# Optimization experiments

Hardware: AMD Instinct MI355X
Metric: run time of the kernel (lower is better)

## Reference

```python
import jax, jax.numpy as jnp
import numpy as np
import math

B, H, N, D = 2, 16, 8192, 64
NUM_PROJS = 7
BLOCK = 256   # key block size
SAMPLE = 256  # number of sampled columns


def _gray_perm(n):
    # AngularLSH._unit_hamming_distance_array: Gray-code ordering of 2**n buckets
    a = np.array([0, 1], dtype=np.int32)
    for i in range(1, n):
        a = np.concatenate([a, a[::-1] + 2 ** i])
    return a

PERM = jnp.asarray(_gray_perm(NUM_PROJS))
ENC = jnp.asarray(2 ** np.arange(NUM_PROJS), dtype=jnp.int32)


def lsh_hash(x, proj_dir):
    # sign-bit angular LSH, then Gray-code remap so nearby buckets share bits
    bits = (jnp.einsum('bhnd,dr->bhnr', x, proj_dir) > 0).astype(jnp.int32)
    bin_ids = (bits * ENC).sum(-1)
    return PERM[bin_ids]


def take_seq(x, idx):
    # gather along the sequence axis (axis=2); idx is [B,H,M]
    return jnp.take_along_axis(x, idx[..., None], axis=2)


def setup_inputs() -> dict:
    key = jax.random.key(0)
    ks = jax.random.split(key, 5)
    return {
        'query': jax.random.normal(ks[0], (B, H, N, D), jnp.float32),
        'key': jax.random.normal(ks[1], (B, H, N, D), jnp.float32),
        'value': jax.random.normal(ks[2], (B, H, N, D), jnp.float32),
        'proj_dir': jax.random.normal(ks[3], (D + 1, NUM_PROJS), jnp.float32),
        'sampled_set': jax.random.randint(ks[4], (B, H, SAMPLE), 0, N),
    }


def reference(query, key, value, proj_dir, sampled_set):
    scale = D ** -0.5

    # asymmetric MIPS transform: key gets sqrt(max||k||^2 - ||k||^2), query gets 0
    k_norm = jnp.linalg.norm(key, axis=-1)                 # [B,H,N]
    k_max = jnp.max(k_norm, axis=-1, keepdims=True)        # [B,H,1]
    k_extra = jnp.sqrt(jnp.maximum(k_max ** 2 - k_norm ** 2, 0.0))
    key_aug = jnp.concatenate([key, k_extra[..., None]], axis=-1)
    query_aug = jnp.concatenate([query, jnp.zeros_like(query[..., :1])], axis=-1)

    # stable sort by LSH bucket; inverse permutation to un-sort queries at the end
    q_idx = jnp.argsort(lsh_hash(query_aug, proj_dir), axis=2, stable=True)
    k_idx = jnp.argsort(lsh_hash(key_aug, proj_dir), axis=2, stable=True)
    q_idx_inv = jnp.argsort(q_idx, axis=2, stable=True)

    q_s = take_seq(query, q_idx)
    k_s = take_seq(key, k_idx)
    v_s = take_seq(value, k_idx)

    nb = N // BLOCK      # number of key blocks (N divisible by BLOCK here)
    qbs = N // nb        # query block size

    # 1) block-diagonal exact attention over LSH-sorted blocks
    qb = q_s.reshape(B, H, nb, qbs, D)
    kb = k_s.reshape(B, H, nb, BLOCK, D)
    vb = v_s.reshape(B, H, nb, BLOCK, D)
    s_blk = jnp.einsum('bhgqd,bhgkd->bhgqk', qb, kb) * scale
    lse_blk = jax.nn.logsumexp(s_blk, axis=-1)             # [B,H,nb,qbs]
    attn_blk = jnp.einsum('bhgqk,bhgkd->bhgqd', jax.nn.softmax(s_blk, axis=-1), vb)
    attn_blk = attn_blk.reshape(B, H, N, D)
    lse_blk = lse_blk.reshape(B, H, N, 1)

    # 2) residual via uniformly sampled columns; mask out columns already in the
    #    query's own diagonal block to avoid double counting
    k_sub = take_seq(k_s, sampled_set)                     # [B,H,S,D]
    v_sub = take_seq(v_s, sampled_set)
    q_blk_id = jnp.arange(N) // qbs                        # [N]
    covered = q_blk_id[None, None, :, None] == (sampled_set // BLOCK)[:, :, None, :]
    bias = jnp.where(covered, jnp.finfo(q_s.dtype).min, 0.0)
    s_res = jnp.einsum('bhnd,bhsd->bhns', q_s, k_sub) * scale + bias
    # importance weight n_key/sample_size applied in log-space (approximate_unsampled)
    lse_res = jax.nn.logsumexp(s_res, axis=-1, keepdims=True) + math.log(N / SAMPLE)
    attn_res = jnp.einsum('bhns,bhsd->bhnd', jax.nn.softmax(s_res, axis=-1), v_sub)

    # add_self_attentions: merge the two softmax estimates in log-space
    c = 1.0 / (1.0 + jnp.exp(lse_res - lse_blk))
    attn = c * attn_blk + (1.0 - c) * attn_res

    # un-sort rows back to the original query order
    attn = take_seq(attn, q_idx_inv)
    return attn
```

## Files before the change

kernel.cpp:

```cpp
#include <hip/hip_runtime.h>
#include <hip/hip_bf16.h>
#include <math.h>

#define BD 2
#define HD 16
#define NSEQ 8192
#define DDIM 64
#define NPROJ 7
#define KBLK 256
#define NSAMP 256
#define NBH (BD*HD)
#define NB (NSEQ/KBLK)

typedef short bf16x8 __attribute__((ext_vector_type(8)));
typedef short bf16x4 __attribute__((ext_vector_type(4)));
typedef float f32x4 __attribute__((ext_vector_type(4)));

__device__ __forceinline__ unsigned int pk2bf(float a, float b) {
    union { __hip_bfloat162 h; unsigned int u; } t;
    t.h = __float22bfloat162_rn(make_float2(a, b));
    return t.u;
}

__global__ __launch_bounds__(256) void prelude_kernel(const float* __restrict__ q,
                                                      const float* __restrict__ k,
                                                      const float* __restrict__ pd,
                                                      float* __restrict__ kdots,
                                                      unsigned int* __restrict__ kmax_bits,
                                                      unsigned char* __restrict__ qh) {
    __shared__ float pds[(DDIM+1)*NPROJ];
    __shared__ float red[256];
    const int tid = threadIdx.x;
    for (int i = tid; i < (DDIM+1)*NPROJ; i += 256) pds[i] = pd[i];
    __syncthreads();

    const int lin = blockIdx.x * 256 + tid;
    const int bh = lin >> 13;

    float acc[NPROJ];
    float4 xv[16];

    {
        const float4* xp = (const float4*)(q + (size_t)lin * DDIM);
        #pragma unroll
        for (int j = 0; j < 16; ++j) xv[j] = xp[j];
        #pragma unroll
        for (int r = 0; r < NPROJ; ++r) acc[r] = 0.f;
        #pragma unroll
        for (int j = 0; j < 16; ++j) {
            float xs[4] = {xv[j].x, xv[j].y, xv[j].z, xv[j].w};
            #pragma unroll
            for (int c = 0; c < 4; ++c) {
                const int d = j*4 + c;
                #pragma unroll
                for (int r = 0; r < NPROJ; ++r) acc[r] += xs[c] * pds[d*NPROJ + r];
            }
        }
        int bin = 0;
        #pragma unroll
        for (int r = 0; r < NPROJ; ++r) bin |= (acc[r] > 0.f) << r;
        qh[lin] = (unsigned char)(bin ^ (bin >> 1));
    }

    float nr;
    {
        const float4* xp = (const float4*)(k + (size_t)lin * DDIM);
        #pragma unroll
        for (int j = 0; j < 16; ++j) xv[j] = xp[j];
        #pragma unroll
        for (int r = 0; r < NPROJ; ++r) acc[r] = 0.f;
        #pragma unroll
        for (int j = 0; j < 16; ++j) {
            float xs[4] = {xv[j].x, xv[j].y, xv[j].z, xv[j].w};
            #pragma unroll
            for (int c = 0; c < 4; ++c) {
                const int d = j*4 + c;
                #pragma unroll
                for (int r = 0; r < NPROJ; ++r) acc[r] += xs[c] * pds[d*NPROJ + r];
            }
        }
        float ss = 0.f;
        #pragma unroll
        for (int j = 0; j < 16; ++j) {
            float4 t = xv[j];
            ss += t.x*t.x + t.y*t.y + t.z*t.z + t.w*t.w;
        }
        nr = sqrtf(ss);
        float4* kd = (float4*)(kdots + (size_t)lin * 8);
        kd[0] = make_float4(acc[0], acc[1], acc[2], acc[3]);
        kd[1] = make_float4(acc[4], acc[5], acc[6], nr);
    }

    red[tid] = nr;
    __syncthreads();
    for (int s = 128; s > 0; s >>= 1) {
        if (tid < s) red[tid] = fmaxf(red[tid], red[tid+s]);
        __syncthreads();
    }
    if (tid == 0) atomicMax(&kmax_bits[bh], __float_as_uint(red[0]));
}

__global__ __launch_bounds__(256) void khash_kernel(const float* __restrict__ pd,
                                                    const float* __restrict__ kdots,
                                                    const unsigned int* __restrict__ kmax_bits,
                                                    unsigned char* __restrict__ kh) {
    const int lin = blockIdx.x * 256 + threadIdx.x;
    const int bh = lin >> 13;
    const float4* kd = (const float4*)(kdots + (size_t)lin * 8);
    float4 d0 = kd[0], d1 = kd[1];
    float acc[NPROJ] = {d0.x, d0.y, d0.z, d0.w, d1.x, d1.y, d1.z};
    const float kn = d1.w;
    const float km = __uint_as_float(kmax_bits[bh]);
    const float ex = sqrtf(fmaxf(km*km - kn*kn, 0.f));
    int bin = 0;
    #pragma unroll
    for (int r = 0; r < NPROJ; ++r) {
        acc[r] += ex * pd[DDIM*NPROJ + r];
        bin |= (acc[r] > 0.f) << r;
    }
    kh[lin] = (unsigned char)(bin ^ (bin >> 1));
}

__global__ __launch_bounds__(256) void sort_kernel(const unsigned char* __restrict__ qhash,
                                                   const unsigned char* __restrict__ khash,
                                                   int* __restrict__ qidx,
                                                   int* __restrict__ kidx) {
    __shared__ unsigned char hsh[NSEQ];
    __shared__ unsigned short cnt[128][264];
    __shared__ int base[128];
    __shared__ int wtot[2];
    const int bh = blockIdx.x, tid = threadIdx.x;
    const unsigned char* hash = blockIdx.y ? khash : qhash;
    int* idx = blockIdx.y ? kidx : qidx;

    {
        const uint4* src = (const uint4*)(hash + (size_t)bh * NSEQ);
        uint4* hdst = (uint4*)hsh;
        hdst[tid] = src[tid];
        hdst[tid + 256] = src[tid + 256];
        unsigned int* cz = (unsigned int*)&cnt[0][0];
        for (int i = tid; i < 128*264/2; i += 256) cz[i] = 0;
    }
    __syncthreads();
    {
        const unsigned char* s = hsh + tid*32;
        for (int i = 0; i < 32; ++i) cnt[s[i]][tid]++;
    }
    __syncthreads();

    int sc = 0, vv = 0;
    if (tid < 128) {
        unsigned run = 0;
        uint4* rp = (uint4*)cnt[tid];
        for (int wd = 0; wd < 32; ++wd) {
            uint4 x = rp[wd];
            unsigned v0 = x.x & 0xffffu, v1 = x.x >> 16;
            unsigned v2 = x.y & 0xffffu, v3 = x.y >> 16;
            unsigned v4 = x.z & 0xffffu, v5 = x.z >> 16;
            unsigned v6 = x.w & 0xffffu, v7 = x.w >> 16;
            unsigned p0 = run, p1 = p0+v0, p2 = p1+v1, p3 = p2+v2,
                     p4 = p3+v3, p5 = p4+v4, p6 = p5+v5, p7 = p6+v6;
            run = p7 + v7;
            x.x = p0 | (p1<<16); x.y = p2 | (p3<<16);
            x.z = p4 | (p5<<16); x.w = p6 | (p7<<16);
            rp[wd] = x;
        }
        vv = (int)run;
        sc = vv;
        #pragma unroll
        for (int d = 1; d < 64; d <<= 1) {
            int t = __shfl_up(sc, d, 64);
            if ((tid & 63) >= d) sc += t;
        }
        if ((tid & 63) == 63) wtot[tid >> 6] = sc;
    }
    __syncthreads();
    if (tid < 128) base[tid] = (sc - vv) + (tid >= 64 ? wtot[0] : 0);
    __syncthreads();
    {
        int* dst = idx + (size_t)bh * NSEQ;
        const unsigned char* s = hsh + tid*32;
        for (int i = 0; i < 32; ++i) {
            int h = s[i];
            int c = cnt[h][tid];
            cnt[h][tid] = (unsigned short)(c + 1);
            dst[base[h] + c] = tid*32 + i;
        }
    }
}

#define VSWZ(d) ((((d) >> 1) & 7) << 4)

__global__ __launch_bounds__(256) void respack_kernel(const float* __restrict__ k,
                                                      const float* __restrict__ v,
                                                      const int* __restrict__ samp,
                                                      const int* __restrict__ kidx,
                                                      char* __restrict__ kres,
                                                      char* __restrict__ vres) {
    const int bh = blockIdx.x, ch = blockIdx.y, tid = threadIdx.x;
    const size_t basef = (size_t)bh * NSEQ * DDIM;
    char* kimg = kres + (size_t)(bh*4 + ch) * 8192;
    char* vimg = vres + (size_t)(bh*4 + ch) * 8192;

    {
        const int kk = tid & 63, dc = tid >> 6;
        const int sp = samp[bh*NSAMP + ch*64 + kk];
        const int row = kidx[bh*NSEQ + sp];
        const float* kr = k + basef + (size_t)row*DDIM + dc*16;
        float4 f0 = ((const float4*)kr)[0], f1 = ((const float4*)kr)[1];
        float4 f2 = ((const float4*)kr)[2], f3 = ((const float4*)kr)[3];
        union { bf16x8 v8; unsigned int u[4]; } h0, h1;
        h0.u[0] = pk2bf(f0.x,f0.y); h0.u[1] = pk2bf(f0.z,f0.w);
        h0.u[2] = pk2bf(f1.x,f1.y); h0.u[3] = pk2bf(f1.z,f1.w);
        h1.u[0] = pk2bf(f2.x,f2.y); h1.u[1] = pk2bf(f2.z,f2.w);
        h1.u[2] = pk2bf(f3.x,f3.y); h1.u[3] = pk2bf(f3.z,f3.w);
        const int rb = kk*128 + dc*32, sw = (kk & 7) << 4;
        *(bf16x8*)(kimg + ((rb) ^ sw)) = h0.v8;
        *(bf16x8*)(kimg + ((rb + 16) ^ sw)) = h1.v8;
    }
    {
        const int vg = tid & 15, kq = tid >> 4;
        const int r0 = kidx[bh*NSEQ + samp[bh*NSAMP + ch*64 + kq*4 + 0]];
        const int r1 = kidx[bh*NSEQ + samp[bh*NSAMP + ch*64 + kq*4 + 1]];
        const int r2 = kidx[bh*NSEQ + samp[bh*NSAMP + ch*64 + kq*4 + 2]];
        const int r3 = kidx[bh*NSEQ + samp[bh*NSAMP + ch*64 + kq*4 + 3]];
        float4 x0 = *(const float4*)(v + basef + (size_t)r0*DDIM + vg*4);
        float4 x1 = *(const float4*)(v + basef + (size_t)r1*DDIM + vg*4);
        float4 x2 = *(const float4*)(v + basef + (size_t)r2*DDIM + vg*4);
        float4 x3 = *(const float4*)(v + basef + (size_t)r3*DDIM + vg*4);
        const float c0[4] = {x0.x, x0.y, x0.z, x0.w};
        const float c1[4] = {x1.x, x1.y, x1.z, x1.w};
        const float c2[4] = {x2.x, x2.y, x2.z, x2.w};
        const float c3[4] = {x3.x, x3.y, x3.z, x3.w};
        #pragma unroll
        for (int j = 0; j < 4; ++j) {
            const int d = vg*4 + j;
            unsigned h01 = pk2bf(c0[j], c1[j]);
            unsigned h23 = pk2bf(c2[j], c3[j]);
            *(uint2*)(vimg + ((d*128 + kq*8) ^ VSWZ(d))) = make_uint2(h01, h23);
        }
    }
}


#define LN32 3.46573590279972f

template<int PHASE>
__device__ __forceinline__ void compute_chunk(
    int ch, int lane,
    const bf16x8 (&qhf)[4][2], const bf16x8 (&qlf)[4][2],
    f32x4 (&O)[4][4], float (&lacc)[4],
    const float* maskF, const char* KhL, const char* VthL) {

    const int lr4 = lane >> 4;
    const int lc  = lane & 15;

    #pragma unroll
    for (int mt = 0; mt < 4; ++mt) {
        const int key = mt*16 + lc;
        const int ksw = (key & 7) << 4;
        bf16x8 ka0 = *(const bf16x8*)(KhL + ((key*128 +  0 + lr4*16) ^ ksw));
        bf16x8 ka1 = *(const bf16x8*)(KhL + ((key*128 + 64 + lr4*16) ^ ksw));
        float4 mk;
        if (PHASE) mk = *(const float4*)(maskF + ch*64 + mt*16 + lr4*4);

        bf16x4 pb[4];
        #pragma unroll
        for (int qt = 0; qt < 4; ++qt) {
            f32x4 c = {0.f, 0.f, 0.f, 0.f};
            c = __builtin_amdgcn_mfma_f32_16x16x32_bf16(ka0, qhf[qt][0], c, 0, 0, 0);
            c = __builtin_amdgcn_mfma_f32_16x16x32_bf16(ka0, qlf[qt][0], c, 0, 0, 0);
            c = __builtin_amdgcn_mfma_f32_16x16x32_bf16(ka1, qhf[qt][1], c, 0, 0, 0);
            c = __builtin_amdgcn_mfma_f32_16x16x32_bf16(ka1, qlf[qt][1], c, 0, 0, 0);
            float e0, e1, e2, e3;
            if (PHASE) {
                e0 = __expf(c[0] + LN32) * mk.x;
                e1 = __expf(c[1] + LN32) * mk.y;
                e2 = __expf(c[2] + LN32) * mk.z;
                e3 = __expf(c[3] + LN32) * mk.w;
            } else {
                e0 = __expf(c[0]); e1 = __expf(c[1]);
                e2 = __expf(c[2]); e3 = __expf(c[3]);
            }
            lacc[qt] += (e0+e1) + (e2+e3);
            union { bf16x4 v4; unsigned int u[2]; } pw;
            pw.u[0] = pk2bf(e0, e1);
            pw.u[1] = pk2bf(e2, e3);
            pb[qt] = pw.v4;
        }

        __builtin_amdgcn_s_setprio(1);
        #pragma unroll
        for (int dt = 0; dt < 4; ++dt) {
            const int d = dt*16 + lc;
            bf16x4 va = *(const bf16x4*)(VthL + ((d*128 + mt*32 + lr4*8) ^ VSWZ(d)));
            #pragma unroll
            for (int qt = 0; qt < 4; ++qt)
                O[qt][dt] = __builtin_amdgcn_mfma_f32_16x16x16bf16_1k(va, pb[qt], O[qt][dt], 0, 0, 0);
        }
        __builtin_amdgcn_s_setprio(0);
    }
}

__global__ __launch_bounds__(256, 2) void attn_kernel(const float* __restrict__ q,
                                                      const float* __restrict__ k,
                                                      const float* __restrict__ v,
                                                      const int* __restrict__ samp,
                                                      const int* __restrict__ qidx,
                                                      const int* __restrict__ kidx,
                                                      const char* __restrict__ kres,
                                                      const char* __restrict__ vres,
                                                      float* __restrict__ out) {
    __shared__ __align__(16) char KB[8192];
    __shared__ __align__(16) char VB[8192];
    __shared__ int qidxL[256];
    __shared__ int kidxL[256];
    __shared__ float maskF[256];

    const int g = blockIdx.x, bh = blockIdx.y;
    const int tid = threadIdx.x;
    const int lane = tid & 63, w = tid >> 6;
    const int lr4 = lane >> 4, lc = lane & 15;
    const size_t basef = (size_t)bh * NSEQ * DDIM;

    qidxL[tid] = qidx[bh*NSEQ + g*KBLK + tid];
    kidxL[tid] = kidx[bh*NSEQ + g*KBLK + tid];
    {
        int sp = samp[bh*NSAMP + tid];
        maskF[tid] = ((sp >> 8) == g) ? 0.f : 1.f;
    }
    __syncthreads();

    bf16x8 qhf[4][2], qlf[4][2];
    #pragma unroll
    for (int qt = 0; qt < 4; ++qt) {
        const int qrow = qidxL[w*64 + qt*16 + lc];
        const float* qp = q + basef + (size_t)qrow*DDIM;
        #pragma unroll
        for (int ks = 0; ks < 2; ++ks) {
            const float* p = qp + ks*32 + lr4*8;
            float4 a = *(const float4*)p;
            float4 b = *(const float4*)(p + 4);
            float xs[8] = {a.x,a.y,a.z,a.w,b.x,b.y,b.z,b.w};
            union { bf16x8 v8; unsigned int u[4]; } hv, lv;
            #pragma unroll
            for (int j = 0; j < 4; ++j) {
                float s0 = xs[2*j]   * 0.125f;
                float s1 = xs[2*j+1] * 0.125f;
                unsigned hp = pk2bf(s0, s1);
                hv.u[j] = hp;
                float l0 = s0 - __uint_as_float(hp << 16);
                float l1 = s1 - __uint_as_float(hp & 0xffff0000u);
                lv.u[j] = pk2bf(l0, l1);
            }
            qhf[qt][ks] = hv.v8; qlf[qt][ks] = lv.v8;
        }
    }

    f32x4 O[4][4];
    #pragma unroll
    for (int a = 0; a < 4; ++a)
        #pragma unroll
        for (int b = 0; b < 4; ++b) O[a][b] = (f32x4){0.f,0.f,0.f,0.f};
    float lacc[4] = {0,0,0,0};

    const int kk = tid & 63, dcw = tid >> 6;
    const int vg = tid & 15, kq = tid >> 4;

    for (int ch = 0; ch < 4; ++ch) {
        __syncthreads();
        {
            const int korig = kidxL[ch*64 + kk];
            const float* kr = k + basef + (size_t)korig*DDIM + dcw*16;
            float4 f0 = ((const float4*)kr)[0], f1 = ((const float4*)kr)[1];
            float4 f2 = ((const float4*)kr)[2], f3 = ((const float4*)kr)[3];
            union { bf16x8 v8; unsigned int u[4]; } h0, h1;
            h0.u[0] = pk2bf(f0.x,f0.y); h0.u[1] = pk2bf(f0.z,f0.w);
            h0.u[2] = pk2bf(f1.x,f1.y); h0.u[3] = pk2bf(f1.z,f1.w);
            h1.u[0] = pk2bf(f2.x,f2.y); h1.u[1] = pk2bf(f2.z,f2.w);
            h1.u[2] = pk2bf(f3.x,f3.y); h1.u[3] = pk2bf(f3.z,f3.w);
            const int rb = kk*128 + dcw*32, sw2 = (kk & 7) << 4;
            *(bf16x8*)(KB + ((rb) ^ sw2)) = h0.v8;
            *(bf16x8*)(KB + ((rb + 16) ^ sw2)) = h1.v8;
        }
        {
            const int r0 = kidxL[ch*64 + kq*4 + 0];
            const int r1 = kidxL[ch*64 + kq*4 + 1];
            const int r2 = kidxL[ch*64 + kq*4 + 2];
            const int r3 = kidxL[ch*64 + kq*4 + 3];
            float4 x0 = *(const float4*)(v + basef + (size_t)r0*DDIM + vg*4);
            float4 x1 = *(const float4*)(v + basef + (size_t)r1*DDIM + vg*4);
            float4 x2 = *(const float4*)(v + basef + (size_t)r2*DDIM + vg*4);
            float4 x3 = *(const float4*)(v + basef + (size_t)r3*DDIM + vg*4);
            const float c0[4] = {x0.x, x0.y, x0.z, x0.w};
            const float c1[4] = {x1.x, x1.y, x1.z, x1.w};
            const float c2[4] = {x2.x, x2.y, x2.z, x2.w};
            const float c3[4] = {x3.x, x3.y, x3.z, x3.w};
            #pragma unroll
            for (int j = 0; j < 4; ++j) {
                const int d = vg*4 + j;
                unsigned h01 = pk2bf(c0[j], c1[j]);
                unsigned h23 = pk2bf(c2[j], c3[j]);
                *(uint2*)(VB + ((d*128 + kq*8) ^ VSWZ(d))) = make_uint2(h01, h23);
            }
        }
        __syncthreads();
        compute_chunk<0>(ch, lane, qhf, qlf, O, lacc, maskF, KB, VB);
    }

    for (int ch = 0; ch < 4; ++ch) {
        __syncthreads();
        {
            const char* ksrc = kres + (size_t)(bh*4 + ch) * 8192 + tid*32;
            const char* vsrc = vres + (size_t)(bh*4 + ch) * 8192 + tid*32;
            float4 a0 = ((const float4*)ksrc)[0];
            float4 a1 = ((const float4*)ksrc)[1];
            float4 b0 = ((const float4*)vsrc)[0];
            float4 b1 = ((const float4*)vsrc)[1];
            *(float4*)(KB + tid*32)      = a0;
            *(float4*)(KB + tid*32 + 16) = a1;
            *(float4*)(VB + tid*32)      = b0;
            *(float4*)(VB + tid*32 + 16) = b1;
        }
        __syncthreads();
        compute_chunk<1>(ch, lane, qhf, qlf, O, lacc, maskF, KB, VB);
    }

    #pragma unroll
    for (int qt = 0; qt < 4; ++qt) {
        lacc[qt] += __shfl_xor(lacc[qt], 16, 64);
        lacc[qt] += __shfl_xor(lacc[qt], 32, 64);
        lacc[qt] = 1.f / lacc[qt];
    }
    float* ob = out + basef;
    #pragma unroll
    for (int qt = 0; qt < 4; ++qt) {
        const int orow = qidxL[w*64 + qt*16 + lc];
        const float f = lacc[qt];
        float* p = ob + (size_t)orow*DDIM + lr4*4;
        #pragma unroll
        for (int dt = 0; dt < 4; ++dt) {
            float4 st = make_float4(O[qt][dt][0]*f, O[qt][dt][1]*f,
                                    O[qt][dt][2]*f, O[qt][dt][3]*f);
            *(float4*)(p + dt*16) = st;
        }
    }
}

extern "C" void kernel_launch(void* const* d_in, const int* in_sizes, int n_in,
                              void* d_out, int out_size, void* d_ws, size_t ws_size,
                              hipStream_t stream) {
    const float* q    = (const float*)d_in[0];
    const float* k    = (const float*)d_in[1];
    const float* v    = (const float*)d_in[2];
    const float* pd   = (const float*)d_in[3];
    const int*   samp = (const int*)d_in[4];
    float* out = (float*)d_out;

    char* ws = (char*)d_ws;
    float*         kdots = (float*)(ws + 0);
    int*           qidx  = (int*)(ws + 0);
    int*           kidx  = (int*)(ws + 1048576);
    char*          kres  = ws + 2097152;
    char*          vres  = ws + 3145728;
    unsigned char* qh    = (unsigned char*)(ws + 8388608);
    unsigned char* kh    = (unsigned char*)(ws + 8650752);
    unsigned int*  kmaxb = (unsigned int*)(ws + 8912896);

    hipMemsetAsync(kmaxb, 0, NBH*sizeof(unsigned int), stream);
    hipLaunchKernelGGL(prelude_kernel, dim3(NBH*NSEQ/256), dim3(256), 0, stream,
                       q, k, pd, kdots, kmaxb, qh);
    hipLaunchKernelGGL(khash_kernel, dim3(NBH*NSEQ/256), dim3(256), 0, stream,
                       pd, kdots, kmaxb, kh);
    hipLaunchKernelGGL(sort_kernel, dim3(NBH, 2), dim3(256), 0, stream, qh, kh, qidx, kidx);
    hipLaunchKernelGGL(respack_kernel, dim3(NBH, 4), dim3(256), 0, stream,
                       k, v, samp, kidx, kres, vres);
    hipLaunchKernelGGL(attn_kernel, dim3(NB, NBH), dim3(256), 0, stream,
                       q, k, v, samp, qidx, kidx, kres, vres, out);
}
```

Baseline: 157.5 us.

## Pre-pack sorted K/V into bf16 LDS images and double-buffer async loads

Adds a pack kernel that gathers the LSH-sorted K/V rows, converts them to bf16 and writes them in the swizzled LDS layout into a large workspace. A new attention kernel then streams these images, plus the residual images, into double-buffered shared memory with direct global-to-LDS loads, so the copy of the next chunk overlaps compute on the current one. The aim is to take the scattered gather and conversion out of the attention inner loop. The new path runs only when the workspace holds at least 84 MB, otherwise the old gather path runs. In exchange it adds a kernel launch and an extra full write and read of K/V, and the larger shared-memory footprint may reduce occupancy.

After: 285.8 us. +81.5%, slower.

```diff
diff --git a/kernel.cpp b/kernel.cpp
--- a/kernel.cpp
+++ b/kernel.cpp
@@ -20,6 +20,12 @@
     union { __hip_bfloat162 h; unsigned int u; } t;
     t.h = __float22bfloat162_rn(make_float2(a, b));
     return t.u;
+}
+
+__device__ __forceinline__ void gload16(const void* gsrc, void* lds) {
+    __builtin_amdgcn_global_load_lds(
+        (const __attribute__((address_space(1))) unsigned int*)gsrc,
+        (__attribute__((address_space(3))) unsigned int*)lds, 16, 0, 0);
 }
 
 __global__ __launch_bounds__(256) void prelude_kernel(const float* __restrict__ q,
@@ -191,55 +197,78 @@
 
 #define VSWZ(d) ((((d) >> 1) & 7) << 4)
 
+__device__ __forceinline__ void pack_k_chunk(const float* kbase, const int* rows,
+                                             int tid, char* kimg) {
+    const int kk = tid & 63, dc = tid >> 6;
+    const int row = rows[kk];
+    const float* kr = kbase + (size_t)row*DDIM + dc*16;
+    float4 f0 = ((const float4*)kr)[0], f1 = ((const float4*)kr)[1];
+    float4 f2 = ((const float4*)kr)[2], f3 = ((const float4*)kr)[3];
+    union { bf16x8 v8; unsigned int u[4]; } h0, h1;
+    h0.u[0] = pk2bf(f0.x,f0.y); h0.u[1] = pk2bf(f0.z,f0.w);
+    h0.u[2] = pk2bf(f1.x,f1.y); h0.u[3] = pk2bf(f1.z,f1.w);
+    h1.u[0] = pk2bf(f2.x,f2.y); h1.u[1] = pk2bf(f2.z,f2.w);
+    h1.u[2] = pk2bf(f3.x,f3.y); h1.u[3] = pk2bf(f3.z,f3.w);
+    const int rb = kk*128 + dc*32, sw = (kk & 7) << 4;
+    *(bf16x8*)(kimg + ((rb) ^ sw)) = h0.v8;
+    *(bf16x8*)(kimg + ((rb + 16) ^ sw)) = h1.v8;
+}
+
+__device__ __forceinline__ void pack_v_chunk(const float* vbase, const int* rows,
+                                             int tid, char* vimg) {
+    const int vg = tid & 15, kq = tid >> 4;
+    const int r0 = rows[kq*4 + 0];
+    const int r1 = rows[kq*4 + 1];
+    const int r2 = rows[kq*4 + 2];
+    const int r3 = rows[kq*4 + 3];
+    float4 x0 = *(const float4*)(vbase + (size_t)r0*DDIM + vg*4);
+    float4 x1 = *(const float4*)(vbase + (size_t)r1*DDIM + vg*4);
+    float4 x2 = *(const float4*)(vbase + (size_t)r2*DDIM + vg*4);
+    float4 x3 = *(const float4*)(vbase + (size_t)r3*DDIM + vg*4);
+    const float c0[4] = {x0.x, x0.y, x0.z, x0.w};
+    const float c1[4] = {x1.x, x1.y, x1.z, x1.w};
+    const float c2[4] = {x2.x, x2.y, x2.z, x2.w};
+    const float c3[4] = {x3.x, x3.y, x3.z, x3.w};
+    #pragma unroll
+    for (int j = 0; j < 4; ++j) {
+        const int d = vg*4 + j;
+        unsigned h01 = pk2bf(c0[j], c1[j]);
+        unsigned h23 = pk2bf(c2[j], c3[j]);
+        *(uint2*)(vimg + ((d*128 + kq*8) ^ VSWZ(d))) = make_uint2(h01, h23);
+    }
+}
+
+__global__ __launch_bounds__(256) void pack_kernel(const float* __restrict__ k,
+                                                   const float* __restrict__ v,
+                                                   const int* __restrict__ kidx,
+                                                   char* __restrict__ kimg,
+                                                   char* __restrict__ vimg) {
+    __shared__ int rows[64];
+    const int bh = blockIdx.x, cj = blockIdx.y, tid = threadIdx.x;
+    if (tid < 64) rows[tid] = kidx[bh*NSEQ + cj*64 + tid];
+    __syncthreads();
+    const size_t basef = (size_t)bh * NSEQ * DDIM;
+    char* kdst = kimg + (size_t)(bh*128 + cj) * 8192;
+    char* vdst = vimg + (size_t)(bh*128 + cj) * 8192;
+    pack_k_chunk(k + basef, rows, tid, kdst);
+    pack_v_chunk(v + basef, rows, tid, vdst);
+}
+
 __global__ __launch_bounds__(256) void respack_kernel(const float* __restrict__ k,
                                                       const float* __restrict__ v,
                                                       const int* __restrict__ samp,
                                                       const int* __restrict__ kidx,
                                                       char* __restrict__ kres,
                                                       char* __restrict__ vres) {
+    __shared__ int rows[64];
     const int bh = blockIdx.x, ch = blockIdx.y, tid = threadIdx.x;
+    if (tid < 64) rows[tid] = kidx[bh*NSEQ + samp[bh*NSAMP + ch*64 + tid]];
+    __syncthreads();
     const size_t basef = (size_t)bh * NSEQ * DDIM;
-    char* kimg = kres + (size_t)(bh*4 + ch) * 8192;
-    char* vimg = vres + (size_t)(bh*4 + ch) * 8192;
-
-    {
-        const int kk = tid & 63, dc = tid >> 6;
-        const int sp = samp[bh*NSAMP + ch*64 + kk];
-        const int row = kidx[bh*NSEQ + sp];
-        const float* kr = k + basef + (size_t)row*DDIM + dc*16;
-        float4 f0 = ((const float4*)kr)[0], f1 = ((const float4*)kr)[1];
-        float4 f2 = ((const float4*)kr)[2], f3 = ((const float4*)kr)[3];
-        union { bf16x8 v8; unsigned int u[4]; } h0, h1;
-        h0.u[0] = pk2bf(f0.x,f0.y); h0.u[1] = pk2bf(f0.z,f0.w);
-        h0.u[2] = pk2bf(f1.x,f1.y); h0.u[3] = pk2bf(f1.z,f1.w);
-        h1.u[0] = pk2bf(f2.x,f2.y); h1.u[1] = pk2bf(f2.z,f2.w);
-        h1.u[2] = pk2bf(f3.x,f3.y); h1.u[3] = pk2bf(f3.z,f3.w);
-        const int rb = kk*128 + dc*32, sw = (kk & 7) << 4;
-        *(bf16x8*)(kimg + ((rb) ^ sw)) = h0.v8;
-        *(bf16x8*)(kimg + ((rb + 16) ^ sw)) = h1.v8;
-    }
-    {
-        const int vg = tid & 15, kq = tid >> 4;
-        const int r0 = kidx[bh*NSEQ + samp[bh*NSAMP + ch*64 + kq*4 + 0]];
-        const int r1 = kidx[bh*NSEQ + samp[bh*NSAMP + ch*64 + kq*4 + 1]];
-        const int r2 = kidx[bh*NSEQ + samp[bh*NSAMP + ch*64 + kq*4 + 2]];
-        const int r3 = kidx[bh*NSEQ + samp[bh*NSAMP + ch*64 + kq*4 + 3]];
-        float4 x0 = *(const float4*)(v + basef + (size_t)r0*DDIM + vg*4);
-        float4 x1 = *(const float4*)(v + basef + (size_t)r1*DDIM + vg*4);
-        float4 x2 = *(const float4*)(v + basef + (size_t)r2*DDIM + vg*4);
-        float4 x3 = *(const float4*)(v + basef + (size_t)r3*DDIM + vg*4);
-        const float c0[4] = {x0.x, x0.y, x0.z, x0.w};
-        const float c1[4] = {x1.x, x1.y, x1.z, x1.w};
-        const float c2[4] = {x2.x, x2.y, x2.z, x2.w};
-        const float c3[4] = {x3.x, x3.y, x3.z, x3.w};
-        #pragma unroll
-        for (int j = 0; j < 4; ++j) {
-            const int d = vg*4 + j;
-            unsigned h01 = pk2bf(c0[j], c1[j]);
-            unsigned h23 = pk2bf(c2[j], c3[j]);
-            *(uint2*)(vimg + ((d*128 + kq*8) ^ VSWZ(d))) = make_uint2(h01, h23);
-        }
-    }
+    char* kdst = kres + (size_t)(bh*4 + ch) * 8192;
+    char* vdst = vres + (size_t)(bh*4 + ch) * 8192;
+    pack_k_chunk(k + basef, rows, tid, kdst);
+    pack_v_chunk(v + basef, rows, tid, vdst);
 }
 
 
@@ -302,36 +331,10 @@
     }
 }
 
-__global__ __launch_bounds__(256, 2) void attn_kernel(const float* __restrict__ q,
-                                                      const float* __restrict__ k,
-                                                      const float* __restrict__ v,
-                                                      const int* __restrict__ samp,
-                                                      const int* __restrict__ qidx,
-                                                      const int* __restrict__ kidx,
-                                                      const char* __restrict__ kres,
-                                                      const char* __restrict__ vres,
-                                                      float* __restrict__ out) {
-    __shared__ __align__(16) char KB[8192];
-    __shared__ __align__(16) char VB[8192];
-    __shared__ int qidxL[256];
-    __shared__ int kidxL[256];
-    __shared__ float maskF[256];
-
-    const int g = blockIdx.x, bh = blockIdx.y;
-    const int tid = threadIdx.x;
-    const int lane = tid & 63, w = tid >> 6;
+__device__ __forceinline__ void load_q_frags(const float* q, size_t basef,
+                                             const int* qidxL, int w, int lane,
+                                             bf16x8 (&qhf)[4][2], bf16x8 (&qlf)[4][2]) {
     const int lr4 = lane >> 4, lc = lane & 15;
-    const size_t basef = (size_t)bh * NSEQ * DDIM;
-
-    qidxL[tid] = qidx[bh*NSEQ + g*KBLK + tid];
-    kidxL[tid] = kidx[bh*NSEQ + g*KBLK + tid];
-    {
-        int sp = samp[bh*NSAMP + tid];
-        maskF[tid] = ((sp >> 8) == g) ? 0.f : 1.f;
-    }
-    __syncthreads();
-
-    bf16x8 qhf[4][2], qlf[4][2];
     #pragma unroll
     for (int qt = 0; qt < 4; ++qt) {
         const int qrow = qidxL[w*64 + qt*16 + lc];
@@ -356,6 +359,71 @@
             qhf[qt][ks] = hv.v8; qlf[qt][ks] = lv.v8;
         }
     }
+}
+
+__device__ __forceinline__ void write_out(float* out, size_t basef,
+                                          const int* qidxL, int w, int lane,
+                                          f32x4 (&O)[4][4], float (&lacc)[4]) {
+    const int lr4 = lane >> 4, lc = lane & 15;
+    #pragma unroll
+    for (int qt = 0; qt < 4; ++qt) {
+        lacc[qt] += __shfl_xor(lacc[qt], 16, 64);
+        lacc[qt] += __shfl_xor(lacc[qt], 32, 64);
+        lacc[qt] = 1.f / lacc[qt];
+    }
+    float* ob = out + basef;
+    #pragma unroll
+    for (int qt = 0; qt < 4; ++qt) {
+        const int orow = qidxL[w*64 + qt*16 + lc];
+        const float f = lacc[qt];
+        float* p = ob + (size_t)orow*DDIM + lr4*4;
+        #pragma unroll
+        for (int dt = 0; dt < 4; ++dt) {
+            float4 st = make_float4(O[qt][dt][0]*f, O[qt][dt][1]*f,
+                                    O[qt][dt][2]*f, O[qt][dt][3]*f);
+            *(float4*)(p + dt*16) = st;
+        }
+    }
+}
+
+__global__ __launch_bounds__(256, 2) void attn_kernel_img(const float* __restrict__ q,
+                                                          const int* __restrict__ samp,
+                                                          const int* __restrict__ qidx,
+                                                          const char* __restrict__ kimg,
+                                                          const char* __restrict__ vimg,
+                                                          const char* __restrict__ kres,
+                                                          const char* __restrict__ vres,
+                                                          float* __restrict__ out) {
+    __shared__ __align__(16) char KB[2][8192];
+    __shared__ __align__(16) char VB[2][8192];
+    __shared__ int qidxL[256];
+    __shared__ float maskF[256];
+
+    const int g = blockIdx.x, bh = blockIdx.y;
+    const int tid = threadIdx.x;
+    const int lane = tid & 63, w = tid >> 6;
+    const size_t basef = (size_t)bh * NSEQ * DDIM;
+
+    qidxL[tid] = qidx[bh*NSEQ + g*KBLK + tid];
+    {
+        int sp = samp[bh*NSAMP + tid];
+        maskF[tid] = ((sp >> 8) == g) ? 0.f : 1.f;
+    }
+
+    {
+        const char* ks = kimg + (size_t)(bh*128 + g*4) * 8192;
+        const char* vs = vimg + (size_t)(bh*128 + g*4) * 8192;
+        char* kl = KB[0] + w*1024;
+        char* vl = VB[0] + w*1024;
+        gload16(ks + tid*16, kl);
+        gload16(ks + 4096 + tid*16, kl + 4096);
+        gload16(vs + tid*16, vl);
+        gload16(vs + 4096 + tid*16, vl + 4096);
+    }
+    __syncthreads();
+
+    bf16x8 qhf[4][2], qlf[4][2];
+    load_q_frags(q, basef, qidxL, w, lane, qhf, qlf);
 
     f32x4 O[4][4];
     #pragma unroll
@@ -364,50 +432,73 @@
         for (int b = 0; b < 4; ++b) O[a][b] = (f32x4){0.f,0.f,0.f,0.f};
     float lacc[4] = {0,0,0,0};
 
-    const int kk = tid & 63, dcw = tid >> 6;
-    const int vg = tid & 15, kq = tid >> 4;
+    for (int ch = 0; ch < 8; ++ch) {
+        if (ch < 7) {
+            const int nch = ch + 1;
+            const char* ks = (nch < 4) ? kimg + (size_t)(bh*128 + g*4 + nch) * 8192
+                                       : kres + (size_t)(bh*4 + nch - 4) * 8192;
+            const char* vs = (nch < 4) ? vimg + (size_t)(bh*128 + g*4 + nch) * 8192
+                                       : vres + (size_t)(bh*4 + nch - 4) * 8192;
+            char* kl = KB[nch & 1] + w*1024;
+            char* vl = VB[nch & 1] + w*1024;
+            gload16(ks + tid*16, kl);
+            gload16(ks + 4096 + tid*16, kl + 4096);
+            gload16(vs + tid*16, vl);
+            gload16(vs + 4096 + tid*16, vl + 4096);
+        }
+        if (ch < 4) compute_chunk<0>(ch,   lane, qhf, qlf, O, lacc, maskF, KB[ch&1], VB[ch&1]);
+        else        compute_chunk<1>(ch-4, lane, qhf, qlf, O, lacc, maskF, KB[ch&1], VB[ch&1]);
+        __syncthreads();
+    }
+
+    write_out(out, basef, qidxL, w, lane, O, lacc);
+}
+
+__global__ __launch_bounds__(256, 2) void attn_kernel_gather(const float* __restrict__ q,
+                                                             const float* __restrict__ k,
+                                                             const float* __restrict__ v,
+                                                             const int* __restrict__ samp,
+                                                             const int* __restrict__ qidx,
+                                                             const int* __restrict__ kidx,
+                                                             const char* __restrict__ kres,
+                                                             const char* __restrict__ vres,
+                                                             float* __restrict__ out) {
+    __shared__ __align__(16) char KB[8192];
+    __shared__ __align__(16) char VB[8192];
+    __shared__ int qidxL[256];
+    __shared__ int kidxL[256];
+    __shared__ float maskF[256];
+
+    const int g = blockIdx.x, bh = blockIdx.y;
+    const int tid = threadIdx.x;
+    const int lane = tid & 63, w = tid >> 6;
+    const size_t basef = (size_t)bh * NSEQ * DDIM;
+
+    qidxL[tid] = qidx[bh*NSEQ + g*KBLK + tid];
+    kidxL[tid] = kidx[bh*NSEQ + g*KBLK + tid];
+    {
+        int sp = samp[bh*NSAMP + tid];
+        maskF[tid] = ((sp >> 8) == g) ? 0.f : 1.f;
+    }
+    __syncthreads();
+
+    bf16x8 qhf[4][2], qlf[4][2];
+    load_q_frags(q, basef, qidxL, w, lane, qhf, qlf);
+
+    f32x4 O[4][4];
+    #pragma unroll
+    for (int a = 0; a < 4; ++a)
+        #pragma unroll
+        for (int b = 0; b < 4; ++b) O[a][b] = (f32x4){0.f,0.f,0.f,0.f};
+    float lacc[4] = {0,0,0,0};
 
     for (int ch = 0; ch < 4; ++ch) {
         __syncthreads();
-        {
-            const int korig = kidxL[ch*64 + kk];
-            const float* kr = k + basef + (size_t)korig*DDIM + dcw*16;
-            float4 f0 = ((const float4*)kr)[0], f1 = ((const float4*)kr)[1];
-            float4 f2 = ((const float4*)kr)[2], f3 = ((const float4*)kr)[3];
-            union { bf16x8 v8; unsigned int u[4]; } h0, h1;
-            h0.u[0] = pk2bf(f0.x,f0.y); h0.u[1] = pk2bf(f0.z,f0.w);
-            h0.u[2] = pk2bf(f1.x,f1.y); h0.u[3] = pk2bf(f1.z,f1.w);
-            h1.u[0] = pk2bf(f2.x,f2.y); h1.u[1] = pk2bf(f2.z,f2.w);
-            h1.u[2] = pk2bf(f3.x,f3.y); h1.u[3] = pk2bf(f3.z,f3.w);
-            const int rb = kk*128 + dcw*32, sw2 = (kk & 7) << 4;
-            *(bf16x8*)(KB + ((rb) ^ sw2)) = h0.v8;
-            *(bf16x8*)(KB + ((rb + 16) ^ sw2)) = h1.v8;
-        }
-        {
-            const int r0 = kidxL[ch*64 + kq*4 + 0];
-            const int r1 = kidxL[ch*64 + kq*4 + 1];
-            const int r2 = kidxL[ch*64 + kq*4 + 2];
-            const int r3 = kidxL[ch*64 + kq*4 + 3];
-            float4 x0 = *(const float4*)(v + basef + (size_t)r0*DDIM + vg*4);
-            float4 x1 = *(const float4*)(v + basef + (size_t)r1*DDIM + vg*4);
-            float4 x2 = *(const float4*)(v + basef + (size_t)r2*DDIM + vg*4);
-            float4 x3 = *(const float4*)(v + basef + (size_t)r3*DDIM + vg*4);
-            const float c0[4] = {x0.x, x0.y, x0.z, x0.w};
-            const float c1[4] = {x1.x, x1.y, x1.z, x1.w};
-            const float c2[4] = {x2.x, x2.y, x2.z, x2.w};
-            const float c3[4] = {x3.x, x3.y, x3.z, x3.w};
-            #pragma unroll
-            for (int j = 0; j < 4; ++j) {
-                const int d = vg*4 + j;
-                unsigned h01 = pk2bf(c0[j], c1[j]);
-                unsigned h23 = pk2bf(c2[j], c3[j]);
-                *(uint2*)(VB + ((d*128 + kq*8) ^ VSWZ(d))) = make_uint2(h01, h23);
-            }
-        }
+        pack_k_chunk(k + basef, kidxL + ch*64, tid, KB);
+        pack_v_chunk(v + basef, kidxL + ch*64, tid, VB);
         __syncthreads();
         compute_chunk<0>(ch, lane, qhf, qlf, O, lacc, maskF, KB, VB);
     }
-
     for (int ch = 0; ch < 4; ++ch) {
         __syncthreads();
         {
@@ -426,25 +517,7 @@
         compute_chunk<1>(ch, lane, qhf, qlf, O, lacc, maskF, KB, VB);
     }
 
-    #pragma unroll
-    for (int qt = 0; qt < 4; ++qt) {
-        lacc[qt] += __shfl_xor(lacc[qt], 16, 64);
-        lacc[qt] += __shfl_xor(lacc[qt], 32, 64);
-        lacc[qt] = 1.f / lacc[qt];
-    }
-    float* ob = out + basef;
-    #pragma unroll
-    for (int qt = 0; qt < 4; ++qt) {
-        const int orow = qidxL[w*64 + qt*16 + lc];
-        const float f = lacc[qt];
-        float* p = ob + (size_t)orow*DDIM + lr4*4;
-        #pragma unroll
-        for (int dt = 0; dt < 4; ++dt) {
-            float4 st = make_float4(O[qt][dt][0]*f, O[qt][dt][1]*f,
-                                    O[qt][dt][2]*f, O[qt][dt][3]*f);
-            *(float4*)(p + dt*16) = st;
-        }
-    }
+    write_out(out, basef, qidxL, w, lane, O, lacc);
 }
 
 extern "C" void kernel_launch(void* const* d_in, const int* in_sizes, int n_in,
@@ -458,23 +531,51 @@
     float* out = (float*)d_out;
 
     char* ws = (char*)d_ws;
-    float*         kdots = (float*)(ws + 0);
-    int*           qidx  = (int*)(ws + 0);
-    int*           kidx  = (int*)(ws + 1048576);
-    char*          kres  = ws + 2097152;
-    char*          vres  = ws + 3145728;
-    unsigned char* qh    = (unsigned char*)(ws + 8388608);
-    unsigned char* kh    = (unsigned char*)(ws + 8650752);
-    unsigned int*  kmaxb = (unsigned int*)(ws + 8912896);
-
-    hipMemsetAsync(kmaxb, 0, NBH*sizeof(unsigned int), stream);
-    hipLaunchKernelGGL(prelude_kernel, dim3(NBH*NSEQ/256), dim3(256), 0, stream,
-                       q, k, pd, kdots, kmaxb, qh);
-    hipLaunchKernelGGL(khash_kernel, dim3(NBH*NSEQ/256), dim3(256), 0, stream,
-                       pd, kdots, kmaxb, kh);
-    hipLaunchKernelGGL(sort_kernel, dim3(NBH, 2), dim3(256), 0, stream, qh, kh, qidx, kidx);
-    hipLaunchKernelGGL(respack_kernel, dim3(NBH, 4), dim3(256), 0, stream,
-                       k, v, samp, kidx, kres, vres);
-    hipLaunchKernelGGL(attn_kernel, dim3(NB, NBH), dim3(256), 0, stream,
-                       q, k, v, samp, qidx, kidx, kres, vres, out);
-}
+    const bool big = ws_size >= (size_t)84 * 1024 * 1024;
+
+    if (big) {
+        int*           qidx  = (int*)(ws + 0);
+        int*           kidx  = (int*)(ws + (1<<20));
+        float*         kdots = (float*)(ws + (2<<20));
+        unsigned char* qh    = (unsigned char*)(ws + (10<<20));
+        unsigned char* kh    = (unsigned char*)(ws + (10<<20) + 262144);
+        unsigned int*  kmaxb = (unsigned int*)(ws + (11<<20));
+        char*          kimg  = ws + ((size_t)16<<20);
+        char*          vimg  = ws + ((size_t)48<<20);
+        char*          kres  = ws + ((size_t)80<<20);
+        char*          vres  = ws + ((size_t)81<<20);
+
+        hipMemsetAsync(kmaxb, 0, NBH*sizeof(unsigned int), stream);
+        hipLaunchKernelGGL(prelude_kernel, dim3(NBH*NSEQ/256), dim3(256), 0, stream,
+                           q, k, pd, kdots, kmaxb, qh);
+        hipLaunchKernelGGL(khash_kernel, dim3(NBH*NSEQ/256), dim3(256), 0, stream,
+                           pd, kdots, kmaxb, kh);
+        hipLaunchKernelGGL(sort_kernel, dim3(NBH, 2), dim3(256), 0, stream, qh, kh, qidx, kidx);
+        hipLaunchKernelGGL(pack_kernel, dim3(NBH, 128), dim3(256), 0, stream,
+                           k, v, kidx, kimg, vimg);
+        hipLaunchKernelGGL(respack_kernel, dim3(NBH, 4), dim3(256), 0, stream,
+                           k, v, samp, kidx, kres, vres);
+        hipLaunchKernelGGL(attn_kernel_img, dim3(NB, NBH), dim3(256), 0, stream,
+                           q, samp, qidx, kimg, vimg, kres, vres, out);
+    } else {
+        float*         kdots = (float*)(ws + 0);
+        int*           qidx  = (int*)(ws + 0);
+        int*           kidx  = (int*)(ws + 1048576);
+        char*          kres  = ws + 2097152;
+        char*          vres  = ws + 3145728;
+        unsigned char* qh    = (unsigned char*)(ws + 8388608);
+        unsigned char* kh    = (unsigned char*)(ws + 8650752);
+        unsigned int*  kmaxb = (unsigned int*)(ws + 8912896);
+
+        hipMemsetAsync(kmaxb, 0, NBH*sizeof(unsigned int), stream);
+        hipLaunchKernelGGL(prelude_kernel, dim3(NBH*NSEQ/256), dim3(256), 0, stream,
+                           q, k, pd, kdots, kmaxb, qh);
+        hipLaunchKernelGGL(khash_kernel, dim3(NBH*NSEQ/256), dim3(256), 0, stream,
+                           pd, kdots, kmaxb, kh);
+        hipLaunchKernelGGL(sort_kernel, dim3(NBH, 2), dim3(256), 0, stream, qh, kh, qidx, kidx);
+        hipLaunchKernelGGL(respack_kernel, dim3(NBH, 4), dim3(256), 0, stream,
+                           k, v, samp, kidx, kres, vres);
+        hipLaunchKernelGGL(attn_kernel_gather, dim3(NB, NBH), dim3(256), 0, stream,
+                           q, k, v, samp, qidx, kidx, kres, vres, out);
+    }
+}
```

## Split attention block across 8 waves with 32 query rows each

Applied to the files above, without the earlier changes.

The attention kernel now launches 512 threads per block, so each wave handles 32 query rows instead of 64. Per-thread register arrays for Q fragments, accumulators and row sums are halved, and the K/V staging loads are redistributed over twice as many threads. This aims to raise occupancy and latency hiding, at the cost of each K/V tile in shared memory being reused by fewer query rows per wave. The residual pack kernel also gathers its sampled row indices once into shared memory instead of re-reading the two-level index per thread.

Result: slower. 168.2 us (+6.8%).

```diff
diff --git a/kernel.cpp b/kernel.cpp
--- a/kernel.cpp
+++ b/kernel.cpp
@@ -197,16 +197,17 @@
                                                       const int* __restrict__ kidx,
                                                       char* __restrict__ kres,
                                                       char* __restrict__ vres) {
+    __shared__ int rows[64];
     const int bh = blockIdx.x, ch = blockIdx.y, tid = threadIdx.x;
+    if (tid < 64) rows[tid] = kidx[bh*NSEQ + samp[bh*NSAMP + ch*64 + tid]];
+    __syncthreads();
     const size_t basef = (size_t)bh * NSEQ * DDIM;
     char* kimg = kres + (size_t)(bh*4 + ch) * 8192;
     char* vimg = vres + (size_t)(bh*4 + ch) * 8192;
 
     {
         const int kk = tid & 63, dc = tid >> 6;
-        const int sp = samp[bh*NSAMP + ch*64 + kk];
-        const int row = kidx[bh*NSEQ + sp];
-        const float* kr = k + basef + (size_t)row*DDIM + dc*16;
+        const float* kr = k + basef + (size_t)rows[kk]*DDIM + dc*16;
         float4 f0 = ((const float4*)kr)[0], f1 = ((const float4*)kr)[1];
         float4 f2 = ((const float4*)kr)[2], f3 = ((const float4*)kr)[3];
         union { bf16x8 v8; unsigned int u[4]; } h0, h1;
@@ -220,10 +221,8 @@
     }
     {
         const int vg = tid & 15, kq = tid >> 4;
-        const int r0 = kidx[bh*NSEQ + samp[bh*NSAMP + ch*64 + kq*4 + 0]];
-        const int r1 = kidx[bh*NSEQ + samp[bh*NSAMP + ch*64 + kq*4 + 1]];
-        const int r2 = kidx[bh*NSEQ + samp[bh*NSAMP + ch*64 + kq*4 + 2]];
-        const int r3 = kidx[bh*NSEQ + samp[bh*NSAMP + ch*64 + kq*4 + 3]];
+        const int r0 = rows[kq*4 + 0], r1 = rows[kq*4 + 1];
+        const int r2 = rows[kq*4 + 2], r3 = rows[kq*4 + 3];
         float4 x0 = *(const float4*)(v + basef + (size_t)r0*DDIM + vg*4);
         float4 x1 = *(const float4*)(v + basef + (size_t)r1*DDIM + vg*4);
         float4 x2 = *(const float4*)(v + basef + (size_t)r2*DDIM + vg*4);
@@ -248,8 +247,8 @@
 template<int PHASE>
 __device__ __forceinline__ void compute_chunk(
     int ch, int lane,
-    const bf16x8 (&qhf)[4][2], const bf16x8 (&qlf)[4][2],
-    f32x4 (&O)[4][4], float (&lacc)[4],
+    const bf16x8 (&qhf)[2][2], const bf16x8 (&qlf)[2][2],
+    f32x4 (&O)[2][4], float (&lacc)[2],
     const float* maskF, const char* KhL, const char* VthL) {
 
     const int lr4 = lane >> 4;
@@ -264,9 +263,9 @@
         float4 mk;
         if (PHASE) mk = *(const float4*)(maskF + ch*64 + mt*16 + lr4*4);
 
-        bf16x4 pb[4];
-        #pragma unroll
-        for (int qt = 0; qt < 4; ++qt) {
+        bf16x4 pb[2];
+        #pragma unroll
+        for (int qt = 0; qt < 2; ++qt) {
             f32x4 c = {0.f, 0.f, 0.f, 0.f};
             c = __builtin_amdgcn_mfma_f32_16x16x32_bf16(ka0, qhf[qt][0], c, 0, 0, 0);
             c = __builtin_amdgcn_mfma_f32_16x16x32_bf16(ka0, qlf[qt][0], c, 0, 0, 0);
@@ -295,14 +294,14 @@
             const int d = dt*16 + lc;
             bf16x4 va = *(const bf16x4*)(VthL + ((d*128 + mt*32 + lr4*8) ^ VSWZ(d)));
             #pragma unroll
-            for (int qt = 0; qt < 4; ++qt)
+            for (int qt = 0; qt < 2; ++qt)
                 O[qt][dt] = __builtin_amdgcn_mfma_f32_16x16x16bf16_1k(va, pb[qt], O[qt][dt], 0, 0, 0);
         }
         __builtin_amdgcn_s_setprio(0);
     }
 }
 
-__global__ __launch_bounds__(256, 2) void attn_kernel(const float* __restrict__ q,
+__global__ __launch_bounds__(512, 4) void attn_kernel(const float* __restrict__ q,
                                                       const float* __restrict__ k,
                                                       const float* __restrict__ v,
                                                       const int* __restrict__ samp,
@@ -315,7 +314,7 @@
     __shared__ __align__(16) char VB[8192];
     __shared__ int qidxL[256];
     __shared__ int kidxL[256];
-    __shared__ float maskF[256];
+    __shared__ __align__(16) float maskF[256];
 
     const int g = blockIdx.x, bh = blockIdx.y;
     const int tid = threadIdx.x;
@@ -323,18 +322,18 @@
     const int lr4 = lane >> 4, lc = lane & 15;
     const size_t basef = (size_t)bh * NSEQ * DDIM;
 
-    qidxL[tid] = qidx[bh*NSEQ + g*KBLK + tid];
-    kidxL[tid] = kidx[bh*NSEQ + g*KBLK + tid];
-    {
+    if (tid < 256) {
+        qidxL[tid] = qidx[bh*NSEQ + g*KBLK + tid];
+        kidxL[tid] = kidx[bh*NSEQ + g*KBLK + tid];
         int sp = samp[bh*NSAMP + tid];
         maskF[tid] = ((sp >> 8) == g) ? 0.f : 1.f;
     }
     __syncthreads();
 
-    bf16x8 qhf[4][2], qlf[4][2];
-    #pragma unroll
-    for (int qt = 0; qt < 4; ++qt) {
-        const int qrow = qidxL[w*64 + qt*16 + lc];
+    bf16x8 qhf[2][2], qlf[2][2];
+    #pragma unroll
+    for (int qt = 0; qt < 2; ++qt) {
+        const int qrow = qidxL[w*32 + qt*16 + lc];
         const float* qp = q + basef + (size_t)qrow*DDIM;
         #pragma unroll
         for (int ks = 0; ks < 2; ++ks) {
@@ -357,51 +356,39 @@
         }
     }
 
-    f32x4 O[4][4];
-    #pragma unroll
-    for (int a = 0; a < 4; ++a)
+    f32x4 O[2][4];
+    #pragma unroll
+    for (int a = 0; a < 2; ++a)
         #pragma unroll
         for (int b = 0; b < 4; ++b) O[a][b] = (f32x4){0.f,0.f,0.f,0.f};
-    float lacc[4] = {0,0,0,0};
-
-    const int kk = tid & 63, dcw = tid >> 6;
-    const int vg = tid & 15, kq = tid >> 4;
+    float lacc[2] = {0,0};
+
+    const int kk = tid & 63, dck = tid >> 6;
+    const int vg = tid & 15, m = tid >> 4;
 
     for (int ch = 0; ch < 4; ++ch) {
         __syncthreads();
         {
             const int korig = kidxL[ch*64 + kk];
-            const float* kr = k + basef + (size_t)korig*DDIM + dcw*16;
+            const float* kr = k + basef + (size_t)korig*DDIM + dck*8;
             float4 f0 = ((const float4*)kr)[0], f1 = ((const float4*)kr)[1];
-            float4 f2 = ((const float4*)kr)[2], f3 = ((const float4*)kr)[3];
-            union { bf16x8 v8; unsigned int u[4]; } h0, h1;
-            h0.u[0] = pk2bf(f0.x,f0.y); h0.u[1] = pk2bf(f0.z,f0.w);
-            h0.u[2] = pk2bf(f1.x,f1.y); h0.u[3] = pk2bf(f1.z,f1.w);
-            h1.u[0] = pk2bf(f2.x,f2.y); h1.u[1] = pk2bf(f2.z,f2.w);
-            h1.u[2] = pk2bf(f3.x,f3.y); h1.u[3] = pk2bf(f3.z,f3.w);
-            const int rb = kk*128 + dcw*32, sw2 = (kk & 7) << 4;
-            *(bf16x8*)(KB + ((rb) ^ sw2)) = h0.v8;
-            *(bf16x8*)(KB + ((rb + 16) ^ sw2)) = h1.v8;
+            union { bf16x8 v8; unsigned int u[4]; } h;
+            h.u[0] = pk2bf(f0.x,f0.y); h.u[1] = pk2bf(f0.z,f0.w);
+            h.u[2] = pk2bf(f1.x,f1.y); h.u[3] = pk2bf(f1.z,f1.w);
+            const int rb = kk*128 + dck*16, sw2 = (kk & 7) << 4;
+            *(bf16x8*)(KB + (rb ^ sw2)) = h.v8;
         }
         {
-            const int r0 = kidxL[ch*64 + kq*4 + 0];
-            const int r1 = kidxL[ch*64 + kq*4 + 1];
-            const int r2 = kidxL[ch*64 + kq*4 + 2];
-            const int r3 = kidxL[ch*64 + kq*4 + 3];
+            const int r0 = kidxL[ch*64 + m*2 + 0];
+            const int r1 = kidxL[ch*64 + m*2 + 1];
             float4 x0 = *(const float4*)(v + basef + (size_t)r0*DDIM + vg*4);
             float4 x1 = *(const float4*)(v + basef + (size_t)r1*DDIM + vg*4);
-            float4 x2 = *(const float4*)(v + basef + (size_t)r2*DDIM + vg*4);
-            float4 x3 = *(const float4*)(v + basef + (size_t)r3*DDIM + vg*4);
             const float c0[4] = {x0.x, x0.y, x0.z, x0.w};
             const float c1[4] = {x1.x, x1.y, x1.z, x1.w};
-            const float c2[4] = {x2.x, x2.y, x2.z, x2.w};
-            const float c3[4] = {x3.x, x3.y, x3.z, x3.w};
             #pragma unroll
             for (int j = 0; j < 4; ++j) {
                 const int d = vg*4 + j;
-                unsigned h01 = pk2bf(c0[j], c1[j]);
-                unsigned h23 = pk2bf(c2[j], c3[j]);
-                *(uint2*)(VB + ((d*128 + kq*8) ^ VSWZ(d))) = make_uint2(h01, h23);
+                *(unsigned*)(VB + ((d*128 + m*4) ^ VSWZ(d))) = pk2bf(c0[j], c1[j]);
             }
         }
         __syncthreads();
@@ -411,31 +398,27 @@
     for (int ch = 0; ch < 4; ++ch) {
         __syncthreads();
         {
-            const char* ksrc = kres + (size_t)(bh*4 + ch) * 8192 + tid*32;
-            const char* vsrc = vres + (size_t)(bh*4 + ch) * 8192 + tid*32;
-            float4 a0 = ((const float4*)ksrc)[0];
-            float4 a1 = ((const float4*)ksrc)[1];
-            float4 b0 = ((const float4*)vsrc)[0];
-            float4 b1 = ((const float4*)vsrc)[1];
-            *(float4*)(KB + tid*32)      = a0;
-            *(float4*)(KB + tid*32 + 16) = a1;
-            *(float4*)(VB + tid*32)      = b0;
-            *(float4*)(VB + tid*32 + 16) = b1;
+            const char* ksrc = kres + (size_t)(bh*4 + ch) * 8192 + tid*16;
+            const char* vsrc = vres + (size_t)(bh*4 + ch) * 8192 + tid*16;
+            float4 a0 = *(const float4*)ksrc;
+            float4 b0 = *(const float4*)vsrc;
+            *(float4*)(KB + tid*16) = a0;
+            *(float4*)(VB + tid*16) = b0;
         }
         __syncthreads();
         compute_chunk<1>(ch, lane, qhf, qlf, O, lacc, maskF, KB, VB);
     }
 
     #pragma unroll
-    for (int qt = 0; qt < 4; ++qt) {
+    for (int qt = 0; qt < 2; ++qt) {
         lacc[qt] += __shfl_xor(lacc[qt], 16, 64);
         lacc[qt] += __shfl_xor(lacc[qt], 32, 64);
         lacc[qt] = 1.f / lacc[qt];
     }
     float* ob = out + basef;
     #pragma unroll
-    for (int qt = 0; qt < 4; ++qt) {
-        const int orow = qidxL[w*64 + qt*16 + lc];
+    for (int qt = 0; qt < 2; ++qt) {
+        const int orow = qidxL[w*32 + qt*16 + lc];
         const float f = lacc[qt];
         float* p = ob + (size_t)orow*DDIM + lr4*4;
         #pragma unroll
@@ -475,6 +458,6 @@
     hipLaunchKernelGGL(sort_kernel, dim3(NBH, 2), dim3(256), 0, stream, qh, kh, qidx, kidx);
     hipLaunchKernelGGL(respack_kernel, dim3(NBH, 4), dim3(256), 0, stream,
                        k, v, samp, kidx, kres, vres);
-    hipLaunchKernelGGL(attn_kernel, dim3(NB, NBH), dim3(256), 0, stream,
+    hipLaunchKernelGGL(attn_kernel, dim3(NB, NBH), dim3(512), 0, stream,
                        q, k, v, samp, qidx, kidx, kres, vres, out);
 }
```
